# Performance work log

Measured on AMD Instinct MI355X. Metric: run time of the kernel, lower is better.

## Reference

```python
import jax, jax.numpy as jnp
import numpy as np

NUM_CLASSES = 5
B, D, H, W = 4, 64, 256, 256


def _per_class_counts(labels, weights, num_classes):
    # labels: [B, N] int, weights: [B, N] float -> [B, C] float counts
    b = labels.shape[0]
    ids = labels + jnp.arange(b, dtype=labels.dtype)[:, None] * num_classes
    counts = jax.ops.segment_sum(weights.ravel(), ids.ravel().astype(jnp.int32),
                                 num_segments=b * num_classes)
    return counts.reshape(b, num_classes)


def _dice(predicted, target, num_classes):
    b = predicted.shape[0]
    p = predicted.reshape(b, -1)  # [B, N] integer class labels
    t = target.reshape(b, -1)
    ones = jnp.ones(p.shape, dtype=jnp.float32)
    pred_sum = _per_class_counts(p, ones, num_classes)                      # sum of one-hot(pred) over voxels
    tar_sum = _per_class_counts(t, ones, num_classes)                       # sum of one-hot(target) over voxels
    inter = _per_class_counts(p, (p == t).astype(jnp.float32), num_classes) # per-class intersection counts
    num = 2.0 * inter
    den = pred_sum + tar_sum
    zero = den == 0
    num = jnp.where(zero, 1.0, num)
    den = jnp.where(zero, 1.0, den)
    return (num / den).mean(axis=0)  # [C]


def setup_inputs() -> dict:
    key = jax.random.key(0)
    k1, k2 = jax.random.split(key)
    predicted = jax.random.randint(k1, (B, D, H, W), 0, NUM_CLASSES, dtype=jnp.int32)
    target = jax.random.randint(k2, (B, D, H, W), 0, NUM_CLASSES, dtype=jnp.int32)
    return {"predicted": predicted, "target": target}


def reference(predicted, target):
    return _dice(predicted, target, NUM_CLASSES)
```

## Files before the change

### kernel.cpp

```cpp
#include <hip/hip_runtime.h>

#define NUM_CLASSES 5
#define BATCH 4
#define NPB (64 * 256 * 256)
#define VEC_PER_BATCH (NPB / 4)
#define THREADS 256
#define VECS 16
#define CHUNK 8
#define BLOCKS_X (VEC_PER_BATCH / (THREADS * VECS))
#define SLOTS 15
#define PSTRIDE 16


__global__ __launch_bounds__(THREADS, 4) void dice_count_kernel(
    const int* __restrict__ pred, const int* __restrict__ targ,
    unsigned int* __restrict__ partial) {
  const int b = blockIdx.y;
  const int4* __restrict__ p4 = (const int4*)(pred + (long long)b * NPB);
  const int4* __restrict__ t4 = (const int4*)(targ + (long long)b * NPB);

  const int base = blockIdx.x * (THREADS * VECS) + threadIdx.x;

  unsigned accP[2] = {0, 0}, accT[2] = {0, 0}, accI[2] = {0, 0};

#pragma unroll
  for (int h = 0; h < 2; ++h) {
    int4 pv[CHUNK], tv[CHUNK];
#pragma unroll
    for (int k = 0; k < CHUNK; ++k) {
      const int idx = base + (h * CHUNK + k) * THREADS;
      pv[k] = p4[idx];
      tv[k] = t4[idx];
    }
    __builtin_amdgcn_sched_barrier(0);
    unsigned aP = 0, aT = 0, aI = 0;
#define ACC_ELEM(PE, TE)                               \
    {                                                  \
      const unsigned op = 1u << (6u * (unsigned)(PE)); \
      aP += op;                                        \
      aT += 1u << (6u * (unsigned)(TE));               \
      aI += ((PE) == (TE)) ? op : 0u;                  \
    }
#pragma unroll
    for (int k = 0; k < CHUNK; ++k) {
      ACC_ELEM(pv[k].x, tv[k].x)
      ACC_ELEM(pv[k].y, tv[k].y)
      ACC_ELEM(pv[k].z, tv[k].z)
      ACC_ELEM(pv[k].w, tv[k].w)
    }
    accP[h] = aP; accT[h] = aT; accI[h] = aI;
  }

#define UNPACK(A, R01, R23, R4)                                          \
  unsigned R01 = ((A[0] & 63u) + (A[1] & 63u)) |                         \
                 ((((A[0] >> 6) & 63u) + ((A[1] >> 6) & 63u)) << 16);    \
  unsigned R23 = (((A[0] >> 12) & 63u) + ((A[1] >> 12) & 63u)) |         \
                 ((((A[0] >> 18) & 63u) + ((A[1] >> 18) & 63u)) << 16);  \
  unsigned R4 = ((A[0] >> 24) & 63u) + ((A[1] >> 24) & 63u);
  UNPACK(accP, p01, p23, p4r)
  UNPACK(accT, t01, t23, t4r)
  UNPACK(accI, i01, i23, i4r)

#pragma unroll
  for (int off = 32; off >= 1; off >>= 1) {
    p01 += (unsigned)__shfl_xor((int)p01, off);
    p23 += (unsigned)__shfl_xor((int)p23, off);
    p4r += (unsigned)__shfl_xor((int)p4r, off);
    t01 += (unsigned)__shfl_xor((int)t01, off);
    t23 += (unsigned)__shfl_xor((int)t23, off);
    t4r += (unsigned)__shfl_xor((int)t4r, off);
    i01 += (unsigned)__shfl_xor((int)i01, off);
    i23 += (unsigned)__shfl_xor((int)i23, off);
    i4r += (unsigned)__shfl_xor((int)i4r, off);
  }

  __shared__ unsigned int s[SLOTS];
  if (threadIdx.x < SLOTS) s[threadIdx.x] = 0;
  __syncthreads();

  if ((threadIdx.x & 63) == 0) {
    atomicAdd(&s[0], p01 & 0xFFFFu);
    atomicAdd(&s[1], p01 >> 16);
    atomicAdd(&s[2], p23 & 0xFFFFu);
    atomicAdd(&s[3], p23 >> 16);
    atomicAdd(&s[4], p4r);
    atomicAdd(&s[5], t01 & 0xFFFFu);
    atomicAdd(&s[6], t01 >> 16);
    atomicAdd(&s[7], t23 & 0xFFFFu);
    atomicAdd(&s[8], t23 >> 16);
    atomicAdd(&s[9], t4r);
    atomicAdd(&s[10], i01 & 0xFFFFu);
    atomicAdd(&s[11], i01 >> 16);
    atomicAdd(&s[12], i23 & 0xFFFFu);
    atomicAdd(&s[13], i23 >> 16);
    atomicAdd(&s[14], i4r);
  }
  __syncthreads();

  if (threadIdx.x < SLOTS)
    partial[(b * BLOCKS_X + blockIdx.x) * PSTRIDE + threadIdx.x] = s[threadIdx.x];
}

__global__ __launch_bounds__(256) void dice_final_kernel(
    const unsigned int* __restrict__ partial, float* __restrict__ out) {
  __shared__ unsigned int red[BATCH * SLOTS][4];
  const int t = threadIdx.x;
  if (t < BATCH * SLOTS * 4) {
    const int q = t & 3;
    const int s = (t >> 2) % SLOTS;
    const int bb = (t >> 2) / SLOTS;
    unsigned int sum = 0;
    for (int j = q * (BLOCKS_X / 4); j < (q + 1) * (BLOCKS_X / 4); ++j)
      sum += partial[(bb * BLOCKS_X + j) * PSTRIDE + s];
    red[(t >> 2)][q] = sum;
  }
  __syncthreads();
  if (t < NUM_CLASSES) {
    float acc = 0.0f;
#pragma unroll
    for (int bb = 0; bb < BATCH; ++bb) {
      const int ip = bb * SLOTS + t;
      const int it = bb * SLOTS + 5 + t;
      const int ii = bb * SLOTS + 10 + t;
      const float ps = (float)(red[ip][0] + red[ip][1] + red[ip][2] + red[ip][3]);
      const float ts = (float)(red[it][0] + red[it][1] + red[it][2] + red[it][3]);
      const float is = (float)(red[ii][0] + red[ii][1] + red[ii][2] + red[ii][3]);
      float num = 2.0f * is;
      float den = ps + ts;
      if (den == 0.0f) { num = 1.0f; den = 1.0f; }
      acc += num / den;
    }
    out[t] = acc * (1.0f / BATCH);
  }
}

extern "C" void kernel_launch(void* const* d_in, const int* in_sizes, int n_in,
                              void* d_out, int out_size, void* d_ws, size_t ws_size,
                              hipStream_t stream) {
  const int* pred = (const int*)d_in[0];
  const int* targ = (const int*)d_in[1];
  float* out = (float*)d_out;
  unsigned int* partial = (unsigned int*)d_ws;

  dim3 grid(BLOCKS_X, BATCH);
  dice_count_kernel<<<grid, THREADS, 0, stream>>>(pred, targ, partial);
  dice_final_kernel<<<1, 256, 0, stream>>>(partial, out);
}
```

Baseline: 147.8 us.

## Software-pipeline vector loads with inline asm and explicit vmcnt waits

Replaces the two-phase load-then-compute structure with a rolling pipeline of six in-flight load pairs. Loads are issued via inline global_load_dwordx4 asm and consumed after s_waitcnt vmcnt, with a new load issued after each chunk is consumed. This keeps memory requests continuously outstanding instead of draining between halves, and uses fewer registers than holding eight pairs at once. Hand-managed waitcnt is fragile: the counts must match the issued loads exactly, or correctness breaks.

```diff
diff --git a/kernel.cpp b/kernel.cpp
--- a/kernel.cpp
+++ b/kernel.cpp
@@ -6,50 +6,75 @@
 #define VEC_PER_BATCH (NPB / 4)
 #define THREADS 256
 #define VECS 16
-#define CHUNK 8
+#define DEPTH 6
 #define BLOCKS_X (VEC_PER_BATCH / (THREADS * VECS))
 #define SLOTS 15
 #define PSTRIDE 16
+
+typedef int vint4 __attribute__((ext_vector_type(4)));
 
 
 __global__ __launch_bounds__(THREADS, 4) void dice_count_kernel(
     const int* __restrict__ pred, const int* __restrict__ targ,
     unsigned int* __restrict__ partial) {
   const int b = blockIdx.y;
-  const int4* __restrict__ p4 = (const int4*)(pred + (long long)b * NPB);
-  const int4* __restrict__ t4 = (const int4*)(targ + (long long)b * NPB);
+  const vint4* __restrict__ p4 = (const vint4*)(pred + (long long)b * NPB);
+  const vint4* __restrict__ t4 = (const vint4*)(targ + (long long)b * NPB);
 
   const int base = blockIdx.x * (THREADS * VECS) + threadIdx.x;
 
+  vint4 pv[DEPTH], tv[DEPTH];
+
+#define ISSUE(J)                                                            \
+  {                                                                         \
+    const void* ap_ = (const void*)(p4 + base + (J) * THREADS);             \
+    const void* at_ = (const void*)(t4 + base + (J) * THREADS);             \
+    asm volatile("global_load_dwordx4 %0, %1, off"                          \
+                 : "=v"(pv[(J) % DEPTH]) : "v"(ap_) : "memory");            \
+    asm volatile("global_load_dwordx4 %0, %1, off"                          \
+                 : "=v"(tv[(J) % DEPTH]) : "v"(at_) : "memory");            \
+  }
+
+#define WAITP(N, J)                                                         \
+  asm volatile("s_waitcnt vmcnt(" #N ")"                                    \
+               : "+v"(pv[(J) % DEPTH]), "+v"(tv[(J) % DEPTH]) :: "memory");
+
   unsigned accP[2] = {0, 0}, accT[2] = {0, 0}, accI[2] = {0, 0};
 
+#define ACC_ELEM(H, PE, TE)                                                 \
+  {                                                                         \
+    const unsigned op = 1u << (6u * (unsigned)(PE));                        \
+    accP[H] += op;                                                          \
+    accT[H] += 1u << (6u * (unsigned)(TE));                                 \
+    accI[H] += ((PE) == (TE)) ? op : 0u;                                    \
+  }
+
+#define PAIRC(J)                                                            \
+  {                                                                         \
+    const int hh = ((J) < 8) ? 0 : 1;                                       \
+    const vint4 pvv = pv[(J) % DEPTH];                                      \
+    const vint4 tvv = tv[(J) % DEPTH];                                      \
+    ACC_ELEM(hh, pvv.x, tvv.x)                                              \
+    ACC_ELEM(hh, pvv.y, tvv.y)                                              \
+    ACC_ELEM(hh, pvv.z, tvv.z)                                              \
+    ACC_ELEM(hh, pvv.w, tvv.w)                                              \
+  }
+
 #pragma unroll
-  for (int h = 0; h < 2; ++h) {
-    int4 pv[CHUNK], tv[CHUNK];
+  for (int j = 0; j < DEPTH; ++j) ISSUE(j)
+
 #pragma unroll
-    for (int k = 0; k < CHUNK; ++k) {
-      const int idx = base + (h * CHUNK + k) * THREADS;
-      pv[k] = p4[idx];
-      tv[k] = t4[idx];
-    }
-    __builtin_amdgcn_sched_barrier(0);
-    unsigned aP = 0, aT = 0, aI = 0;
-#define ACC_ELEM(PE, TE)                               \
-    {                                                  \
-      const unsigned op = 1u << (6u * (unsigned)(PE)); \
-      aP += op;                                        \
-      aT += 1u << (6u * (unsigned)(TE));               \
-      aI += ((PE) == (TE)) ? op : 0u;                  \
-    }
-#pragma unroll
-    for (int k = 0; k < CHUNK; ++k) {
-      ACC_ELEM(pv[k].x, tv[k].x)
-      ACC_ELEM(pv[k].y, tv[k].y)
-      ACC_ELEM(pv[k].z, tv[k].z)
-      ACC_ELEM(pv[k].w, tv[k].w)
-    }
-    accP[h] = aP; accT[h] = aT; accI[h] = aI;
+  for (int j = 0; j < VECS - DEPTH; ++j) {
+    WAITP(10, j)
+    PAIRC(j)
+    ISSUE(j + DEPTH)
   }
+  WAITP(10, 10) PAIRC(10)
+  WAITP(8, 11)  PAIRC(11)
+  WAITP(6, 12)  PAIRC(12)
+  WAITP(4, 13)  PAIRC(13)
+  WAITP(2, 14)  PAIRC(14)
+  WAITP(0, 15)  PAIRC(15)
 
 #define UNPACK(A, R01, R23, R4)                                          \
   unsigned R01 = ((A[0] & 63u) + (A[1] & 63u)) |                         \
```

Measured after the change: 150.3 us. About the same (+1.7%).
